# Optimization experiments

Hardware: AMD Instinct MI355X
Metric: run time of the kernel (lower is better)

The kernel has to match this reference:

```python
import jax, jax.numpy as jnp
import numpy as np

N_NODES = 100000


def setup_inputs() -> dict:
    key = jax.random.key(0)
    ks = jax.random.split(key, 6)
    E = 1600000
    return {
        "features": jax.random.normal(ks[0], (N_NODES, 128), dtype=jnp.float32),
        "W1": jax.random.normal(ks[1], (128, 32), dtype=jnp.float32) * 0.08,
        "b1": jnp.zeros((32,), dtype=jnp.float32),
        "W2": jax.random.normal(ks[2], (32, 32), dtype=jnp.float32) * 0.17,
        "b2": jnp.zeros((32,), dtype=jnp.float32),
        "src": jax.random.randint(ks[3], (E,), 0, N_NODES, dtype=jnp.int32),
        "dst": jax.random.randint(ks[4], (E,), 0, N_NODES, dtype=jnp.int32),
    }


def _graph_conv(x, W, b, src, dst, norm_src, norm_dst, n_nodes):
    # DGL GraphConv, norm='both': project, scale by src norm, aggregate, scale by dst norm
    h = x @ W                                   # [N, F_out]
    msg = h[src] * norm_src[:, None]            # [E, F_out] gather + scale
    agg = jax.ops.segment_sum(msg, dst, num_segments=n_nodes)  # [N, F_out]
    return agg * norm_dst[:, None] + b


def reference(features, W1, b1, W2, b2, src, dst):
    n = features.shape[0]
    ones = jnp.ones(src.shape[0], dtype=features.dtype)
    deg_out = jax.ops.segment_sum(ones, src, num_segments=n)   # out-degree (src side)
    deg_in = jax.ops.segment_sum(ones, dst, num_segments=n)    # in-degree (dst side)
    norm_out = jax.lax.rsqrt(jnp.clip(deg_out, 1.0))
    norm_in = jax.lax.rsqrt(jnp.clip(deg_in, 1.0))
    norm_src = norm_out[src]                                    # per-edge src norm
    h = jax.nn.relu(_graph_conv(features, W1, b1, src, dst, norm_src, norm_in, n))
    return _graph_conv(h, W2, b2, src, dst, norm_src, norm_in, n)
```

## Files before the change

kernel.cpp:

```cpp
#include <hip/hip_runtime.h>
#include <hip/hip_fp16.h>

#define N_NODES 100000
#define F_IN 128
#define F_HID 32
#define BN 512
#define NBUCK 196
#define NBLK 256
#define PART_THREADS 1024
#define STAGE_CAP 12288

typedef _Float16 f16x8 __attribute__((ext_vector_type(8)));
typedef float f32x4 __attribute__((ext_vector_type(4)));


__global__ __launch_bounds__(PART_THREADS) void part_count(const int* __restrict__ src,
                                                           const int* __restrict__ dst, int E,
                                                           unsigned* __restrict__ cntD,
                                                           unsigned* __restrict__ cntS) {
    __shared__ unsigned cd[NBUCK], cs[NBUCK];
    for (int i = threadIdx.x; i < NBUCK; i += PART_THREADS) { cd[i] = 0; cs[i] = 0; }
    __syncthreads();
    int chunk = (E + NBLK - 1) / NBLK;
    int e0 = blockIdx.x * chunk, e1 = min(E, e0 + chunk);
    for (int e = e0 + threadIdx.x; e < e1; e += PART_THREADS) {
        atomicAdd(&cd[((unsigned)dst[e]) >> 9], 1u);
        atomicAdd(&cs[((unsigned)src[e]) >> 9], 1u);
    }
    __syncthreads();
    unsigned* od = cntD + (size_t)blockIdx.x * NBUCK;
    unsigned* os = cntS + (size_t)blockIdx.x * NBUCK;
    for (int i = threadIdx.x; i < NBUCK; i += PART_THREADS) { od[i] = cd[i]; os[i] = cs[i]; }
}

__global__ __launch_bounds__(NBLK) void col_scan2(unsigned* __restrict__ cntD,
                                                  unsigned* __restrict__ cntS,
                                                  unsigned* __restrict__ totD,
                                                  unsigned* __restrict__ totS) {
    __shared__ unsigned buf[2][NBLK];
    bool isD = blockIdx.x < NBUCK;
    unsigned* cnt = isD ? cntD : cntS;
    unsigned* totals = isD ? totD : totS;
    int k = isD ? blockIdx.x : blockIdx.x - NBUCK;
    int t = threadIdx.x;
    unsigned v = cnt[(size_t)t * NBUCK + k];
    buf[0][t] = v;
    __syncthreads();
    int cur = 0;
    for (int off = 1; off < NBLK; off <<= 1) {
        unsigned x = buf[cur][t];
        if (t >= off) x += buf[cur][t - off];
        buf[cur ^ 1][t] = x;
        cur ^= 1;
        __syncthreads();
    }
    cnt[(size_t)t * NBUCK + k] = buf[cur][t] - v;
    if (t == NBLK - 1) totals[k] = buf[cur][NBLK - 1];
}

__global__ __launch_bounds__(1024) void total_scan2(const unsigned* __restrict__ totD,
                                                    const unsigned* __restrict__ totS,
                                                    unsigned* __restrict__ startD,
                                                    unsigned* __restrict__ startS) {
    __shared__ unsigned buf[2][1024];
    const unsigned* totals = (blockIdx.x == 0) ? totD : totS;
    unsigned* start = (blockIdx.x == 0) ? startD : startS;
    int t = threadIdx.x;
    buf[0][t] = (t < NBUCK) ? totals[t] : 0;
    __syncthreads();
    int cur = 0;
    for (int off = 1; off < 1024; off <<= 1) {
        unsigned x = buf[cur][t];
        if (t >= off) x += buf[cur][t - off];
        buf[cur ^ 1][t] = x;
        cur ^= 1;
        __syncthreads();
    }
    if (t < NBUCK) start[t + 1] = buf[cur][t];
    if (t == 0) start[0] = 0;
}

__global__ __launch_bounds__(PART_THREADS) void part_scatter(const int* __restrict__ src,
                                                             const int* __restrict__ dst, int E,
                                                             const unsigned* __restrict__ cntD,
                                                             const unsigned* __restrict__ cntS,
                                                             const unsigned* __restrict__ startD,
                                                             const unsigned* __restrict__ startS,
                                                             unsigned* __restrict__ pairD,
                                                             unsigned short* __restrict__ valS) {
    __shared__ unsigned curD[NBUCK], curS[NBUCK];
    for (int i = threadIdx.x; i < NBUCK; i += PART_THREADS) { curD[i] = 0; curS[i] = 0; }
    __syncthreads();
    int chunk = (E + NBLK - 1) / NBLK;
    int e0 = blockIdx.x * chunk, e1 = min(E, e0 + chunk);
    const unsigned* bd = cntD + (size_t)blockIdx.x * NBUCK;
    const unsigned* bs = cntS + (size_t)blockIdx.x * NBUCK;
    for (int e = e0 + threadIdx.x; e < e1; e += PART_THREADS) {
        unsigned s = (unsigned)src[e], d = (unsigned)dst[e];
        unsigned kd = d >> 9, ks = s >> 9;
        unsigned rd = atomicAdd(&curD[kd], 1u);
        pairD[startD[kd] + bd[kd] + rd] = s | ((d & 511u) << 17);
        unsigned rs = atomicAdd(&curS[ks], 1u);
        valS[startS[ks] + bs[ks] + rs] = (unsigned short)(s & 511u);
    }
}


__global__ __launch_bounds__(512) void sort_norms(const unsigned* __restrict__ pairD,
                                                  const unsigned* __restrict__ startD,
                                                  const unsigned short* __restrict__ valS,
                                                  const unsigned* __restrict__ startS,
                                                  int* __restrict__ col, int* __restrict__ row_ptr,
                                                  int* __restrict__ deg_arr,
                                                  float* __restrict__ norm_in,
                                                  float* __restrict__ norm_out, int n) {
    __shared__ unsigned ed[STAGE_CAP];
    __shared__ unsigned cnt[BN];
    __shared__ unsigned base[BN];
    __shared__ unsigned sbuf[2][BN];
    int t = threadIdx.x;
    if (blockIdx.x < NBUCK) {
        int k = blockIdx.x;
        unsigned a0 = startD[k], a1 = startD[k + 1];
        int tot = (int)(a1 - a0);
        int staged = tot < STAGE_CAP ? tot : STAGE_CAP;
        for (int i = t; i < staged; i += 512) ed[i] = pairD[a0 + i];
        cnt[t] = 0;
        __syncthreads();
        for (int i = t; i < staged; i += 512)
            atomicAdd(&cnt[(ed[i] >> 17) & (BN - 1)], 1u);
        for (int i = staged + t; i < tot; i += 512)
            atomicAdd(&cnt[(pairD[a0 + i] >> 17) & (BN - 1)], 1u);
        __syncthreads();
        unsigned v = cnt[t];
        sbuf[0][t] = v;
        __syncthreads();
        int cur = 0;
        for (int off = 1; off < BN; off <<= 1) {
            unsigned x = sbuf[cur][t];
            if (t >= off) x += sbuf[cur][t - off];
            sbuf[cur ^ 1][t] = x;
            cur ^= 1;
            __syncthreads();
        }
        base[t] = a0 + sbuf[cur][t] - v;
        int node = k * BN + t;
        if (node < n) {
            row_ptr[node] = (int)base[t];
            deg_arr[node] = (int)v;
            norm_in[node] = rsqrtf((float)(v > 1u ? v : 1u));
        }
        cnt[t] = 0;
        __syncthreads();
        for (int i = t; i < staged; i += 512) {
            unsigned pv = ed[i];
            unsigned l = (pv >> 17) & (BN - 1);
            unsigned r = atomicAdd(&cnt[l], 1u);
            col[base[l] + r] = (int)(pv & 0x1FFFFu);
        }
        for (int i = staged + t; i < tot; i += 512) {
            unsigned pv = pairD[a0 + i];
            unsigned l = (pv >> 17) & (BN - 1);
            unsigned r = atomicAdd(&cnt[l], 1u);
            col[base[l] + r] = (int)(pv & 0x1FFFFu);
        }
    } else {
        int k = blockIdx.x - NBUCK;
        cnt[t] = 0;
        __syncthreads();
        unsigned a0 = startS[k], a1 = startS[k + 1];
        for (unsigned i = a0 + t; i < a1; i += 512)
            atomicAdd(&cnt[valS[i]], 1u);
        __syncthreads();
        int node = k * BN + t;
        if (node < n) {
            unsigned c = cnt[t];
            norm_out[node] = rsqrtf((float)(c > 1u ? c : 1u));
        }
    }
}


__device__ __forceinline__ float2 pack_half4(float a, float b, float c, float d) {
    __half2 h0 = __floats2half2_rn(a, b);
    __half2 h1 = __floats2half2_rn(c, d);
    float2 r;
    r.x = *reinterpret_cast<float*>(&h0);
    r.y = *reinterpret_cast<float*>(&h1);
    return r;
}

__device__ __forceinline__ void unpack_half4(float2 v, float4& acc) {
    __half2 ha = *reinterpret_cast<__half2*>(&v.x);
    __half2 hb = *reinterpret_cast<__half2*>(&v.y);
    float2 fa = __half22float2(ha);
    float2 fb = __half22float2(hb);
    acc.x += fa.x; acc.y += fa.y; acc.z += fb.x; acc.w += fb.y;
}


__global__ __launch_bounds__(256) void gemm1_mfma(const float* __restrict__ x,
                                                  const float* __restrict__ W,
                                                  const float* __restrict__ norm_out,
                                                  float2* __restrict__ hh, int n) {
    int lane = threadIdx.x & 63;
    int wv = threadIdx.x >> 6;
    int node0 = blockIdx.x * 64 + wv * 16;
    int m = lane & 15;
    int kg = lane >> 4;
    int node = node0 + m;
    int nodeClamp = node < n ? node : (n - 1);
    const float* xrow = x + (size_t)nodeClamp * F_IN;

    f16x8 bfrag[4];
#pragma unroll
    for (int c = 0; c < 4; ++c) {
        float4 lo = *reinterpret_cast<const float4*>(xrow + c * 32 + kg * 4);
        float4 hi = *reinterpret_cast<const float4*>(xrow + c * 32 + 16 + kg * 4);
        f16x8 b;
        b[0] = (_Float16)lo.x; b[1] = (_Float16)lo.y; b[2] = (_Float16)lo.z; b[3] = (_Float16)lo.w;
        b[4] = (_Float16)hi.x; b[5] = (_Float16)hi.y; b[6] = (_Float16)hi.z; b[7] = (_Float16)hi.w;
        bfrag[c] = b;
    }
    f32x4 acc0 = {0.f, 0.f, 0.f, 0.f};
    f32x4 acc1 = {0.f, 0.f, 0.f, 0.f};
#pragma unroll
    for (int c = 0; c < 4; ++c) {
        f16x8 a0, a1;
#pragma unroll
        for (int j = 0; j < 4; ++j) {
            int k0 = c * 32 + kg * 4 + j;
            int k1 = k0 + 16;
            a0[j]     = (_Float16)W[k0 * F_HID + m];
            a0[j + 4] = (_Float16)W[k1 * F_HID + m];
            a1[j]     = (_Float16)W[k0 * F_HID + 16 + m];
            a1[j + 4] = (_Float16)W[k1 * F_HID + 16 + m];
        }
        acc0 = __builtin_amdgcn_mfma_f32_16x16x32_f16(a0, bfrag[c], acc0, 0, 0, 0);
        acc1 = __builtin_amdgcn_mfma_f32_16x16x32_f16(a1, bfrag[c], acc1, 0, 0, 0);
    }
    if (node < n) {
        float no = norm_out[node];
        hh[(size_t)node * 8 + kg] = pack_half4(acc0[0] * no, acc0[1] * no, acc0[2] * no, acc0[3] * no);
        hh[(size_t)node * 8 + 4 + kg] = pack_half4(acc1[0] * no, acc1[1] * no, acc1[2] * no, acc1[3] * no);
    }
}


__device__ __forceinline__ float4 shfl4_8(float4 v, int sl) {
    float4 r;
    r.x = __shfl(v.x, sl, 8);
    r.y = __shfl(v.y, sl, 8);
    r.z = __shfl(v.z, sl, 8);
    r.w = __shfl(v.w, sl, 8);
    return r;
}

__global__ __launch_bounds__(256) void agg1_kernel(const float2* __restrict__ h1h,
                                                   const int* __restrict__ row_ptr,
                                                   const int* __restrict__ deg_arr,
                                                   const int* __restrict__ col,
                                                   const float* __restrict__ norm_in,
                                                   const float* __restrict__ norm_out,
                                                   const float* __restrict__ b1,
                                                   const float* __restrict__ W2,
                                                   float2* __restrict__ h2h, int n) {
    __shared__ float W2l[F_HID * F_HID];
    for (int i = threadIdx.x; i < F_HID * F_HID; i += 256) W2l[i] = W2[i];
    __syncthreads();
    const float4* W24 = reinterpret_cast<const float4*>(W2l);
    int q = threadIdx.x & 7;
    int node = blockIdx.x * 32 + (threadIdx.x >> 3);
    if (node >= n) return;
    int start = row_ptr[node];
    int deg = deg_arr[node];
    float4 acc = make_float4(0.f, 0.f, 0.f, 0.f);
    int jj = 0;
    for (; jj + 8 <= deg; jj += 8) {
        int c = col[start + jj + q];
#pragma unroll
        for (int m = 0; m < 8; ++m) {
            int s = __shfl(c, m, 8);
            float2 v = h1h[(size_t)s * 8 + q];
            unpack_half4(v, acc);
        }
    }
    int rem = deg - jj;
    if (rem > 0) {
        int c = col[start + jj + (q < rem ? q : 0)];
        for (int m = 0; m < rem; ++m) {
            int s = __shfl(c, m, 8);
            float2 v = h1h[(size_t)s * 8 + q];
            unpack_half4(v, acc);
        }
    }
    float ni = norm_in[node];
    const float4 b14 = reinterpret_cast<const float4*>(b1)[q];
    float4 t;
    t.x = fmaxf(acc.x * ni + b14.x, 0.f);
    t.y = fmaxf(acc.y * ni + b14.y, 0.f);
    t.z = fmaxf(acc.z * ni + b14.z, 0.f);
    t.w = fmaxf(acc.w * ni + b14.w, 0.f);
    float4 o = make_float4(0.f, 0.f, 0.f, 0.f);
#pragma unroll
    for (int sl = 0; sl < 8; ++sl) {
        float4 tt = shfl4_8(t, sl);
        int kb = sl * 4;
        float4 w0 = W24[(kb + 0) * 8 + q];
        float4 w1 = W24[(kb + 1) * 8 + q];
        float4 w2 = W24[(kb + 2) * 8 + q];
        float4 w3 = W24[(kb + 3) * 8 + q];
        o.x += tt.x * w0.x + tt.y * w1.x + tt.z * w2.x + tt.w * w3.x;
        o.y += tt.x * w0.y + tt.y * w1.y + tt.z * w2.y + tt.w * w3.y;
        o.z += tt.x * w0.z + tt.y * w1.z + tt.z * w2.z + tt.w * w3.z;
        o.w += tt.x * w0.w + tt.y * w1.w + tt.z * w2.w + tt.w * w3.w;
    }
    float no = norm_out[node];
    h2h[(size_t)node * 8 + q] = pack_half4(o.x * no, o.y * no, o.z * no, o.w * no);
}

__global__ __launch_bounds__(256) void agg2_kernel(const float2* __restrict__ h2h,
                                                   const int* __restrict__ row_ptr,
                                                   const int* __restrict__ deg_arr,
                                                   const int* __restrict__ col,
                                                   const float* __restrict__ norm_in,
                                                   const float* __restrict__ b2,
                                                   float* __restrict__ out, int n) {
    int q = threadIdx.x & 7;
    int node = blockIdx.x * 32 + (threadIdx.x >> 3);
    if (node >= n) return;
    int start = row_ptr[node];
    int deg = deg_arr[node];
    float4 acc = make_float4(0.f, 0.f, 0.f, 0.f);
    int jj = 0;
    for (; jj + 8 <= deg; jj += 8) {
        int c = col[start + jj + q];
#pragma unroll
        for (int m = 0; m < 8; ++m) {
            int s = __shfl(c, m, 8);
            float2 v = h2h[(size_t)s * 8 + q];
            unpack_half4(v, acc);
        }
    }
    int rem = deg - jj;
    if (rem > 0) {
        int c = col[start + jj + (q < rem ? q : 0)];
        for (int m = 0; m < rem; ++m) {
            int s = __shfl(c, m, 8);
            float2 v = h2h[(size_t)s * 8 + q];
            unpack_half4(v, acc);
        }
    }
    float ni = norm_in[node];
    const float4 b24 = reinterpret_cast<const float4*>(b2)[q];
    float4 o;
    o.x = acc.x * ni + b24.x;
    o.y = acc.y * ni + b24.y;
    o.z = acc.z * ni + b24.z;
    o.w = acc.w * ni + b24.w;
    reinterpret_cast<float4*>(out)[(size_t)node * 8 + q] = o;
}


static inline size_t align256(size_t x) { return (x + 255) & ~(size_t)255; }

extern "C" void kernel_launch(void* const* d_in, const int* in_sizes, int n_in,
                              void* d_out, int out_size, void* d_ws, size_t ws_size,
                              hipStream_t stream) {
    const float* features = (const float*)d_in[0];
    const float* W1 = (const float*)d_in[1];
    const float* b1 = (const float*)d_in[2];
    const float* W2 = (const float*)d_in[3];
    const float* b2 = (const float*)d_in[4];
    const int* src = (const int*)d_in[5];
    const int* dst = (const int*)d_in[6];
    const int E = in_sizes[5];
    const int n = N_NODES;
    float* out = (float*)d_out;

    char* ws = (char*)d_ws;
    size_t off = 0;
    float* norm_out = (float*)(ws + off); off += align256((size_t)n * 4);
    float* norm_in = (float*)(ws + off);  off += align256((size_t)n * 4);
    int* row_ptr = (int*)(ws + off);      off += align256((size_t)n * 4);
    int* deg_arr = (int*)(ws + off);      off += align256((size_t)n * 4);
    unsigned* startD = (unsigned*)(ws + off); off += align256((NBUCK + 1) * 4);
    unsigned* startS = (unsigned*)(ws + off); off += align256((NBUCK + 1) * 4);
    unsigned* totD = (unsigned*)(ws + off);   off += align256(NBUCK * 4);
    unsigned* totS = (unsigned*)(ws + off);   off += align256(NBUCK * 4);
    int* col = (int*)(ws + off);              off += align256((size_t)E * 4);

    size_t regX = off;
    unsigned* pairD = (unsigned*)(ws + regX);
    unsigned short* valS = (unsigned short*)(ws + regX + (size_t)E * 4);
    float2* h2h = (float2*)(ws + regX);
    off += align256((size_t)2 * E * 4);
    size_t regY = off;
    unsigned* cntD = (unsigned*)(ws + regY);
    unsigned* cntS = (unsigned*)(ws + regY + (size_t)NBLK * NBUCK * 4);
    float2* h1h = (float2*)(ws + regY);

    part_count<<<NBLK, PART_THREADS, 0, stream>>>(src, dst, E, cntD, cntS);
    col_scan2<<<2 * NBUCK, NBLK, 0, stream>>>(cntD, cntS, totD, totS);
    total_scan2<<<2, 1024, 0, stream>>>(totD, totS, startD, startS);
    part_scatter<<<NBLK, PART_THREADS, 0, stream>>>(src, dst, E, cntD, cntS, startD, startS,
                                                    pairD, valS);

    sort_norms<<<2 * NBUCK, 512, 0, stream>>>(pairD, startD, valS, startS, col, row_ptr,
                                              deg_arr, norm_in, norm_out, n);

    gemm1_mfma<<<(n + 63) / 64, 256, 0, stream>>>(features, W1, norm_out, h1h, n);

    agg1_kernel<<<(n + 31) / 32, 256, 0, stream>>>(h1h, row_ptr, deg_arr, col, norm_in,
                                                   norm_out, b1, W2, h2h, n);
    agg2_kernel<<<(n + 31) / 32, 256, 0, stream>>>(h2h, row_ptr, deg_arr, col, norm_in, b2, out, n);
}
```

Before: 115.2 us.

## Vectorize edge partition loads and degree-sort nodes within buckets for aggregation

The edge partition count and scatter kernels now read src/dst with int4 vector loads, using chunks aligned to 4 elements. sort_norms additionally builds a per-bucket permutation of nodes ordered by in-degree, using a shared-memory histogram. The two aggregation kernels process nodes in that order so that lanes in a wavefront handle similar-degree nodes, which reduces divergence in the gather loops. In exchange, the kernels take an extra indirection, and their node stores become less contiguous.

```diff
diff --git a/kernel.cpp b/kernel.cpp
--- a/kernel.cpp
+++ b/kernel.cpp
@@ -21,11 +21,19 @@
     __shared__ unsigned cd[NBUCK], cs[NBUCK];
     for (int i = threadIdx.x; i < NBUCK; i += PART_THREADS) { cd[i] = 0; cs[i] = 0; }
     __syncthreads();
-    int chunk = (E + NBLK - 1) / NBLK;
+    int chunk = ((E + NBLK * 4 - 1) / (NBLK * 4)) * 4;
     int e0 = blockIdx.x * chunk, e1 = min(E, e0 + chunk);
-    for (int e = e0 + threadIdx.x; e < e1; e += PART_THREADS) {
-        atomicAdd(&cd[((unsigned)dst[e]) >> 9], 1u);
-        atomicAdd(&cs[((unsigned)src[e]) >> 9], 1u);
+    for (int e = e0 + threadIdx.x * 4; e < e1; e += PART_THREADS * 4) {
+        int4 dv = *reinterpret_cast<const int4*>(dst + e);
+        int4 sv = *reinterpret_cast<const int4*>(src + e);
+        atomicAdd(&cd[((unsigned)dv.x) >> 9], 1u);
+        atomicAdd(&cd[((unsigned)dv.y) >> 9], 1u);
+        atomicAdd(&cd[((unsigned)dv.z) >> 9], 1u);
+        atomicAdd(&cd[((unsigned)dv.w) >> 9], 1u);
+        atomicAdd(&cs[((unsigned)sv.x) >> 9], 1u);
+        atomicAdd(&cs[((unsigned)sv.y) >> 9], 1u);
+        atomicAdd(&cs[((unsigned)sv.z) >> 9], 1u);
+        atomicAdd(&cs[((unsigned)sv.w) >> 9], 1u);
     }
     __syncthreads();
     unsigned* od = cntD + (size_t)blockIdx.x * NBUCK;
@@ -91,17 +99,23 @@
     __shared__ unsigned curD[NBUCK], curS[NBUCK];
     for (int i = threadIdx.x; i < NBUCK; i += PART_THREADS) { curD[i] = 0; curS[i] = 0; }
     __syncthreads();
-    int chunk = (E + NBLK - 1) / NBLK;
+    int chunk = ((E + NBLK * 4 - 1) / (NBLK * 4)) * 4;
     int e0 = blockIdx.x * chunk, e1 = min(E, e0 + chunk);
     const unsigned* bd = cntD + (size_t)blockIdx.x * NBUCK;
     const unsigned* bs = cntS + (size_t)blockIdx.x * NBUCK;
-    for (int e = e0 + threadIdx.x; e < e1; e += PART_THREADS) {
-        unsigned s = (unsigned)src[e], d = (unsigned)dst[e];
-        unsigned kd = d >> 9, ks = s >> 9;
-        unsigned rd = atomicAdd(&curD[kd], 1u);
-        pairD[startD[kd] + bd[kd] + rd] = s | ((d & 511u) << 17);
-        unsigned rs = atomicAdd(&curS[ks], 1u);
-        valS[startS[ks] + bs[ks] + rs] = (unsigned short)(s & 511u);
+    for (int e = e0 + threadIdx.x * 4; e < e1; e += PART_THREADS * 4) {
+        int4 sv = *reinterpret_cast<const int4*>(src + e);
+        int4 dv = *reinterpret_cast<const int4*>(dst + e);
+#pragma unroll
+        for (int u = 0; u < 4; ++u) {
+            unsigned s = (unsigned)((u == 0) ? sv.x : (u == 1) ? sv.y : (u == 2) ? sv.z : sv.w);
+            unsigned d = (unsigned)((u == 0) ? dv.x : (u == 1) ? dv.y : (u == 2) ? dv.z : dv.w);
+            unsigned kd = d >> 9, ks = s >> 9;
+            unsigned rd = atomicAdd(&curD[kd], 1u);
+            pairD[startD[kd] + bd[kd] + rd] = s | ((d & 511u) << 17);
+            unsigned rs = atomicAdd(&curS[ks], 1u);
+            valS[startS[ks] + bs[ks] + rs] = (unsigned short)(s & 511u);
+        }
     }
 }
 
@@ -113,11 +127,13 @@
                                                   int* __restrict__ col, int* __restrict__ row_ptr,
                                                   int* __restrict__ deg_arr,
                                                   float* __restrict__ norm_in,
-                                                  float* __restrict__ norm_out, int n) {
+                                                  float* __restrict__ norm_out,
+                                                  int* __restrict__ perm, int n) {
     __shared__ unsigned ed[STAGE_CAP];
     __shared__ unsigned cnt[BN];
     __shared__ unsigned base[BN];
     __shared__ unsigned sbuf[2][BN];
+    __shared__ unsigned hist[64], hbase[64], hcur[64];
     int t = threadIdx.x;
     if (blockIdx.x < NBUCK) {
         int k = blockIdx.x;
@@ -126,6 +142,7 @@
         int staged = tot < STAGE_CAP ? tot : STAGE_CAP;
         for (int i = t; i < staged; i += 512) ed[i] = pairD[a0 + i];
         cnt[t] = 0;
+        if (t < 64) hist[t] = 0;
         __syncthreads();
         for (int i = t; i < staged; i += 512)
             atomicAdd(&cnt[(ed[i] >> 17) & (BN - 1)], 1u);
@@ -145,13 +162,25 @@
         }
         base[t] = a0 + sbuf[cur][t] - v;
         int node = k * BN + t;
+        unsigned bin = v < 63u ? v : 63u;
         if (node < n) {
             row_ptr[node] = (int)base[t];
             deg_arr[node] = (int)v;
             norm_in[node] = rsqrtf((float)(v > 1u ? v : 1u));
+            atomicAdd(&hist[bin], 1u);
         }
         cnt[t] = 0;
         __syncthreads();
+        if (t == 0) {
+            unsigned run = 0;
+            for (int i = 0; i < 64; ++i) { hbase[i] = run; run += hist[i]; }
+        }
+        if (t < 64) hcur[t] = 0;
+        __syncthreads();
+        if (node < n) {
+            unsigned r = atomicAdd(&hcur[bin], 1u);
+            perm[k * BN + hbase[bin] + r] = node;
+        }
         for (int i = t; i < staged; i += 512) {
             unsigned pv = ed[i];
             unsigned l = (pv >> 17) & (BN - 1);
@@ -260,6 +289,7 @@
                                                    const int* __restrict__ row_ptr,
                                                    const int* __restrict__ deg_arr,
                                                    const int* __restrict__ col,
+                                                   const int* __restrict__ perm,
                                                    const float* __restrict__ norm_in,
                                                    const float* __restrict__ norm_out,
                                                    const float* __restrict__ b1,
@@ -270,8 +300,9 @@
     __syncthreads();
     const float4* W24 = reinterpret_cast<const float4*>(W2l);
     int q = threadIdx.x & 7;
-    int node = blockIdx.x * 32 + (threadIdx.x >> 3);
-    if (node >= n) return;
+    int idx = blockIdx.x * 32 + (threadIdx.x >> 3);
+    if (idx >= n) return;
+    int node = perm[idx];
     int start = row_ptr[node];
     int deg = deg_arr[node];
     float4 acc = make_float4(0.f, 0.f, 0.f, 0.f);
@@ -323,12 +354,14 @@
                                                    const int* __restrict__ row_ptr,
                                                    const int* __restrict__ deg_arr,
                                                    const int* __restrict__ col,
+                                                   const int* __restrict__ perm,
                                                    const float* __restrict__ norm_in,
                                                    const float* __restrict__ b2,
                                                    float* __restrict__ out, int n) {
     int q = threadIdx.x & 7;
-    int node = blockIdx.x * 32 + (threadIdx.x >> 3);
-    if (node >= n) return;
+    int idx = blockIdx.x * 32 + (threadIdx.x >> 3);
+    if (idx >= n) return;
+    int node = perm[idx];
     int start = row_ptr[node];
     int deg = deg_arr[node];
     float4 acc = make_float4(0.f, 0.f, 0.f, 0.f);
@@ -384,6 +417,7 @@
     float* norm_in = (float*)(ws + off);  off += align256((size_t)n * 4);
     int* row_ptr = (int*)(ws + off);      off += align256((size_t)n * 4);
     int* deg_arr = (int*)(ws + off);      off += align256((size_t)n * 4);
+    int* perm = (int*)(ws + off);         off += align256((size_t)n * 4);
     unsigned* startD = (unsigned*)(ws + off); off += align256((NBUCK + 1) * 4);
     unsigned* startS = (unsigned*)(ws + off); off += align256((NBUCK + 1) * 4);
     unsigned* totD = (unsigned*)(ws + off);   off += align256(NBUCK * 4);
@@ -407,11 +441,12 @@
                                                     pairD, valS);
 
     sort_norms<<<2 * NBUCK, 512, 0, stream>>>(pairD, startD, valS, startS, col, row_ptr,
-                                              deg_arr, norm_in, norm_out, n);
+                                              deg_arr, norm_in, norm_out, perm, n);
 
     gemm1_mfma<<<(n + 63) / 64, 256, 0, stream>>>(features, W1, norm_out, h1h, n);
 
-    agg1_kernel<<<(n + 31) / 32, 256, 0, stream>>>(h1h, row_ptr, deg_arr, col, norm_in,
+    agg1_kernel<<<(n + 31) / 32, 256, 0, stream>>>(h1h, row_ptr, deg_arr, col, perm, norm_in,
                                                    norm_out, b1, W2, h2h, n);
-    agg2_kernel<<<(n + 31) / 32, 256, 0, stream>>>(h2h, row_ptr, deg_arr, col, norm_in, b2, out, n);
-}
+    agg2_kernel<<<(n + 31) / 32, 256, 0, stream>>>(h2h, row_ptr, deg_arr, col, perm, norm_in,
+                                                   b2, out, n);
+}
```

After: 123.5 us. +7.3%, slower.
